# Optimization experiments

Hardware: AMD Instinct MI355X
Metric: run time of the kernel (lower is better)

## Reference

```python
import jax, jax.numpy as jnp
import numpy as np

POOL, D_MODEL, D_FF, M_DIM = 512, 1024, 4096, 64
B, S, K = 2, 2048, 8


def setup_inputs() -> dict:
    key = jax.random.key(0)
    ks = jax.random.split(key, 8)
    x = jax.random.normal(ks[0], (B, S, D_MODEL), dtype=jnp.float32)
    selected_indices = jax.random.randint(ks[1], (B, S, K), 0, POOL, dtype=jnp.int32)
    pattern_weights = jax.random.normal(ks[2], (B, S, K), dtype=jnp.float32)
    base_patterns = 0.02 * jax.random.normal(ks[3], (POOL, D_FF), dtype=jnp.float32)
    # nn.Linear(d_model, pool_size*mod_dim): weight [P*M, d_model], xavier-uniform
    lim_cm = float(np.sqrt(6.0 / (D_MODEL + POOL * M_DIM)))
    cm_w = jax.random.uniform(ks[4], (POOL * M_DIM, D_MODEL), jnp.float32, -lim_cm, lim_cm)
    cm_b = jnp.zeros((POOL * M_DIM,), jnp.float32)
    adj_proj = 0.01 * jax.random.normal(ks[5], (M_DIM, D_FF), dtype=jnp.float32)
    lim_w2 = float(np.sqrt(6.0 / (D_FF + D_MODEL)))
    w2_w = jax.random.uniform(ks[6], (D_MODEL, D_FF), jnp.float32, -lim_w2, lim_w2)
    w2_b = jnp.zeros((D_MODEL,), jnp.float32)
    return {"x": x, "selected_indices": selected_indices, "pattern_weights": pattern_weights,
            "base_patterns": base_patterns, "cm_w": cm_w, "cm_b": cm_b,
            "adj_proj": adj_proj, "w2_w": w2_w, "w2_b": w2_b}


def reference(x, selected_indices, pattern_weights, base_patterns, cm_w, cm_b, adj_proj, w2_w, w2_b):
    b, s, k = selected_indices.shape
    # gather base firing patterns for selected neurons: [b,s,k,d_ff]
    bp = base_patterns[selected_indices]
    # dense context modulation then gather (matches original module): [b,s,P,M]
    mod = (jnp.einsum('bsd,nd->bsn', x, cm_w) + cm_b).reshape(b, s, POOL, M_DIM)
    sel_mod = jnp.take_along_axis(mod, selected_indices[..., None], axis=2)  # [b,s,k,M]
    adjustments = jnp.einsum('bskm,mf->bskf', sel_mod, adj_proj)
    adjusted = bp + adjustments  # [b,s,k,d_ff]
    w = jax.nn.softmax(pattern_weights, axis=-1)
    combined = jnp.einsum('bsk,bskf->bsf', w, adjusted)  # [b,s,d_ff]
    activated = jax.nn.gelu(combined, approximate=False)  # torch default gelu = exact erf
    return jnp.einsum('bsf,df->bsd', activated, w2_w) + w2_b
```

## Files before the change

### kernel.cpp

```cpp
#include <hip/hip_runtime.h>
#include <math.h>

#define T_    4096
#define K_    8
#define POOL_ 512
#define DM_   1024
#define DFF_  4096
#define MD_   64
#define KC_   576

typedef __bf16 bf16x8 __attribute__((ext_vector_type(8)));
typedef __bf16 bf16x4 __attribute__((ext_vector_type(4)));
typedef float  f32x4  __attribute__((ext_vector_type(4)));

typedef __attribute__((address_space(1))) const void g_void;
typedef __attribute__((address_space(3))) void s_void;

__device__ __forceinline__ void async_ld16(const void* g, void* s) {
    __builtin_amdgcn_global_load_lds((g_void*)g, (s_void*)s, 16, 0, 0);
}
__device__ __forceinline__ float gelu_exact(float g) {
    return 0.5f * g * (1.f + erff(g * 0.70710678118654752f));
}
__device__ __forceinline__ bf16x4 cvt4(float4 v) {
    bf16x4 o;
    o[0] = (__bf16)v.x; o[1] = (__bf16)v.y; o[2] = (__bf16)v.z; o[3] = (__bf16)v.w;
    return o;
}
__device__ __forceinline__ bf16x8 cvt8(float4 a, float4 b) {
    bf16x8 o;
    o[0] = (__bf16)a.x; o[1] = (__bf16)a.y; o[2] = (__bf16)a.z; o[3] = (__bf16)a.w;
    o[4] = (__bf16)b.x; o[5] = (__bf16)b.y; o[6] = (__bf16)b.z; o[7] = (__bf16)b.w;
    return o;
}

__global__ __launch_bounds__(256) void k_hist(const int* __restrict__ sel,
                                              int* __restrict__ counts) {
    int i = blockIdx.x * 256 + threadIdx.x;
    if (i < T_ * K_) atomicAdd(&counts[sel[i]], 1);
}

__global__ __launch_bounds__(512) void k_scan(const int* __restrict__ counts,
                                              int* __restrict__ offsets,
                                              int* __restrict__ cursor) {
    __shared__ int s[512];
    const int t = threadIdx.x;
    const int c = counts[t];
    s[t] = c;
    __syncthreads();
    for (int d = 1; d < 512; d <<= 1) {
        int v = (t >= d) ? s[t - d] : 0;
        __syncthreads();
        s[t] += v;
        __syncthreads();
    }
    offsets[t] = s[t] - c;
    cursor[t]  = s[t] - c;
    if (t == 511) offsets[512] = s[511];
}

__global__ __launch_bounds__(256) void k_scatter(const int* __restrict__ sel,
                                                 int* __restrict__ cursor,
                                                 int* __restrict__ bucket,
                                                 int* __restrict__ rank) {
    int i = blockIdx.x * 256 + threadIdx.x;
    if (i < T_ * K_) {
        int p = sel[i];
        int pos = atomicAdd(&cursor[p], 1);
        bucket[pos] = i;
        rank[i] = pos;
    }
}

__global__ __launch_bounds__(256) void k_cvt(const float* __restrict__ src,
                                             __bf16* __restrict__ dst, int n16) {
    int i = blockIdx.x * 256 + threadIdx.x;
    if (i >= n16) return;
    const float4* s = (const float4*)src + (long)i * 4;
    float4 a = s[0], b = s[1], c = s[2], d = s[3];
    bf16x8 o0 = cvt8(a, b), o1 = cvt8(c, d);
    bf16x8* dp = (bf16x8*)dst + (long)i * 2;
    dp[0] = o0; dp[1] = o1;
}

__global__ __launch_bounds__(256) void k_selmod(
    const __bf16* __restrict__ xb, const float* __restrict__ cm_w,
    const int* __restrict__ bucket, const int* __restrict__ offsets,
    float* __restrict__ Y)
{
    const int p   = blockIdx.x;
    const int ms  = blockIdx.y;
    const int off = offsets[p];
    const int n   = offsets[p + 1] - off;
    if (n == 0) return;

    const int wave = threadIdx.x >> 6, lane = threadIdx.x & 63;
    const int quad = lane >> 4, l15 = lane & 15;

    const float* wrow = cm_w + (long)(p * 64 + ms * 16 + l15) * DM_ + quad * 8;

    const int nch = (n + 15) >> 4;
    for (int c = wave; c < nch; c += 4) {
        const int base = c * 16;
        int row = base + l15; if (row >= n) row = n - 1;
        const int tok = bucket[off + row] >> 3;
        const __bf16* xrow = xb + (long)tok * DM_ + quad * 8;

        f32x4 acc = {};
        #pragma unroll 4
        for (int kc = 0; kc < DM_; kc += 32) {
            bf16x8 afr = *(const bf16x8*)(xrow + kc);
            float4 w0  = *(const float4*)(wrow + kc);
            float4 w1  = *(const float4*)(wrow + kc + 4);
            bf16x8 bfr = cvt8(w0, w1);
            acc = __builtin_amdgcn_mfma_f32_16x16x32_bf16(afr, bfr, acc, 0, 0, 0);
        }
        #pragma unroll
        for (int r = 0; r < 4; ++r) {
            int prow = base + quad * 4 + r;
            if (prow < n)
                Y[(long)(off + prow) * MD_ + ms * 16 + l15] = acc[r];
        }
    }
}

__global__ __launch_bounds__(256) void k_wdense(
    const float* __restrict__ Y, const int* __restrict__ sel,
    const int* __restrict__ rank, const float* __restrict__ pw,
    const float* __restrict__ cm_b, __bf16* __restrict__ Wd)
{
    const int tid = threadIdx.x;
    const int tt = tid >> 6, m = tid & 63;
    const int t = blockIdx.x * 4 + tt;
    __shared__ float w_s[4][8];
    __shared__ int   sidx[4][8];
    __shared__ int   rnk[4][8];
    __shared__ __align__(16) __bf16 row[4][KC_];

    if (m < 8) {
        w_s[tt][m]  = pw[t * 8 + m];
        sidx[tt][m] = sel[t * 8 + m];
        rnk[tt][m]  = rank[t * 8 + m];
    }
    __syncthreads();
    if (m == 0) {
        float mx = w_s[tt][0];
        #pragma unroll
        for (int k = 1; k < 8; ++k) mx = fmaxf(mx, w_s[tt][k]);
        float sum = 0.f;
        #pragma unroll
        for (int k = 0; k < 8; ++k) { float e = expf(w_s[tt][k] - mx); w_s[tt][k] = e; sum += e; }
        float inv = 1.f / sum;
        #pragma unroll
        for (int k = 0; k < 8; ++k) w_s[tt][k] *= inv;
    }
    __syncthreads();
    *(uint4*)&row[tt][m * 8] = make_uint4(0, 0, 0, 0);
    {
        float a = 0.f;
        #pragma unroll
        for (int k = 0; k < 8; ++k) {
            float y = cm_b[sidx[tt][k] * 64 + m] + Y[(long)rnk[tt][k] * MD_ + m];
            a += w_s[tt][k] * y;
        }
        row[tt][512 + m] = (__bf16)a;
    }
    __syncthreads();
    if (m == 0) {
        #pragma unroll
        for (int k = 0; k < 8; ++k) {
            int c = sidx[tt][k];
            row[tt][c] = (__bf16)((float)row[tt][c] + w_s[tt][k]);
        }
    }
    __syncthreads();
    const uint4* src = (const uint4*)&row[0][0];
    uint4* dst = (uint4*)(Wd + (long)blockIdx.x * 4 * KC_);
    for (int e = tid; e < 4 * KC_ * 2 / 16; e += 256) dst[e] = src[e];
}

__global__ __launch_bounds__(256) void k_buildP(
    const float* __restrict__ bp, const float* __restrict__ adj,
    __bf16* __restrict__ P)
{
    __shared__ __bf16 tile[64][72];
    const int tid = threadIdx.x;
    const int bx = blockIdx.x, f0 = blockIdx.y * 64;
    const float* src = (bx < 8) ? (bp + (long)bx * 64 * DFF_) : adj;
    for (int e = tid; e < 4096; e += 256) {
        int f = e & 63, c = e >> 6;
        tile[c][f] = (__bf16)src[(long)c * DFF_ + f0 + f];
    }
    __syncthreads();
    const int c0 = bx * 64;
    for (int e = tid; e < 4096; e += 256) {
        int c = e & 63, f = e >> 6;
        P[(long)(f0 + f) * KC_ + c0 + c] = tile[c][f];
    }
}

__global__ __launch_bounds__(256) void k_actgemm(
    const __bf16* __restrict__ A, const __bf16* __restrict__ Bw,
    __bf16* __restrict__ act)
{
    __shared__ __align__(16) __bf16 sA[128 * 32];
    __shared__ __align__(16) __bf16 sB[128 * 32];
    const int tid  = threadIdx.x;
    const int tm   = blockIdx.y * 128, tn = blockIdx.x * 128;
    const int wave = tid >> 6, lane = tid & 63, quad = lane >> 4, l15 = lane & 15;
    const int wm   = (wave >> 1) * 64, wn = (wave & 1) * 64;

    f32x4 acc[4][4] = {};

    const int e    = tid * 8;
    const int srow = e >> 5;
    const int scol = e & 31;
    const __bf16* agp0 = A  + ((long)(tm + srow)      * KC_ + scol);
    const __bf16* agp1 = A  + ((long)(tm + 64 + srow) * KC_ + scol);
    const __bf16* bgp0 = Bw + ((long)(tn + srow)      * KC_ + scol);
    const __bf16* bgp1 = Bw + ((long)(tn + 64 + srow) * KC_ + scol);
    void* sa0 = (void*)(sA + e);
    void* sa1 = (void*)(sA + 2048 + e);
    void* sb0 = (void*)(sB + e);
    void* sb1 = (void*)(sB + 2048 + e);

    for (int kk = 0; kk < KC_; kk += 32) {
        async_ld16(agp0 + kk, sa0);
        async_ld16(agp1 + kk, sa1);
        async_ld16(bgp0 + kk, sb0);
        async_ld16(bgp1 + kk, sb1);
        __syncthreads();
        bf16x8 af[4], bf[4];
        #pragma unroll
        for (int i = 0; i < 4; ++i)
            af[i] = *(const bf16x8*)(sA + (wm + i * 16 + l15) * 32 + quad * 8);
        #pragma unroll
        for (int j = 0; j < 4; ++j)
            bf[j] = *(const bf16x8*)(sB + (wn + j * 16 + l15) * 32 + quad * 8);
        #pragma unroll
        for (int i = 0; i < 4; ++i)
            #pragma unroll
            for (int j = 0; j < 4; ++j)
                acc[i][j] = __builtin_amdgcn_mfma_f32_16x16x32_bf16(af[i], bf[j], acc[i][j], 0, 0, 0);
        __syncthreads();
    }

    #pragma unroll
    for (int j = 0; j < 4; ++j) {
        const int col = tn + wn + j * 16 + l15;
        #pragma unroll
        for (int i = 0; i < 4; ++i) {
            const int row = tm + wm + i * 16 + quad * 4;
            #pragma unroll
            for (int r = 0; r < 4; ++r)
                act[(long)(row + r) * DFF_ + col] = (__bf16)gelu_exact(acc[i][j][r]);
        }
    }
}

__global__ __launch_bounds__(256) void k_outgemm(
    const __bf16* __restrict__ A, const __bf16* __restrict__ Bw,
    const float* __restrict__ bias, float* __restrict__ out)
{
    __shared__ __align__(16) __bf16 sA[128 * 128];
    __shared__ __align__(16) __bf16 sB[128 * 128];
    const int tid  = threadIdx.x;
    const int tm   = blockIdx.y * 128, tn = blockIdx.x * 128;
    const int wave = tid >> 6, lane = tid & 63, quad = lane >> 4, l15 = lane & 15;
    const int wm   = (wave >> 1) * 64, wn = (wave & 1) * 64;

    f32x4 acc[4][4] = {};

    const int e  = tid * 8;
    const int r0 = e >> 5;
    const int cc = e & 31;

    for (int kk = 0; kk < DFF_; kk += 128) {
        #pragma unroll
        for (int s = 0; s < 4; ++s) {
            #pragma unroll
            for (int q = 0; q < 2; ++q) {
                async_ld16(A  + (long)(tm + q * 64 + r0) * DFF_ + kk + s * 32 + cc,
                           (void*)(sA + s * 4096 + q * 2048 + e));
                async_ld16(Bw + (long)(tn + q * 64 + r0) * DFF_ + kk + s * 32 + cc,
                           (void*)(sB + s * 4096 + q * 2048 + e));
            }
        }
        __syncthreads();
        #pragma unroll
        for (int s = 0; s < 4; ++s) {
            bf16x8 af[4], bf[4];
            #pragma unroll
            for (int i = 0; i < 4; ++i)
                af[i] = *(const bf16x8*)(sA + s * 4096 + (wm + i * 16 + l15) * 32 + quad * 8);
            #pragma unroll
            for (int j = 0; j < 4; ++j)
                bf[j] = *(const bf16x8*)(sB + s * 4096 + (wn + j * 16 + l15) * 32 + quad * 8);
            #pragma unroll
            for (int i = 0; i < 4; ++i)
                #pragma unroll
                for (int j = 0; j < 4; ++j)
                    acc[i][j] = __builtin_amdgcn_mfma_f32_16x16x32_bf16(af[i], bf[j], acc[i][j], 0, 0, 0);
        }
        __syncthreads();
    }

    #pragma unroll
    for (int j = 0; j < 4; ++j) {
        const int col = tn + wn + j * 16 + l15;
        const float bj = bias[col];
        #pragma unroll
        for (int i = 0; i < 4; ++i) {
            const int row = tm + wm + i * 16 + quad * 4;
            #pragma unroll
            for (int r = 0; r < 4; ++r)
                out[(long)(row + r) * 1024 + col] = acc[i][j][r] + bj;
        }
    }
}

extern "C" void kernel_launch(void* const* d_in, const int* in_sizes, int n_in,
                              void* d_out, int out_size, void* d_ws, size_t ws_size,
                              hipStream_t stream) {
    const float* x    = (const float*)d_in[0];
    const int*   sel  = (const int*)  d_in[1];
    const float* pw   = (const float*)d_in[2];
    const float* bp   = (const float*)d_in[3];
    const float* cm_w = (const float*)d_in[4];
    const float* cm_b = (const float*)d_in[5];
    const float* adj  = (const float*)d_in[6];
    const float* w2   = (const float*)d_in[7];
    const float* w2b  = (const float*)d_in[8];
    float* out = (float*)d_out;

    char* ws = (char*)d_ws;
    __bf16* x_bf = (__bf16*)ws;
    __bf16* act  = (__bf16*)ws;
    __bf16* P    = (__bf16*)(ws + (size_t)32 * 1024 * 1024);
    __bf16* w2bf = (__bf16*)(ws + (size_t)37 * 1024 * 1024);
    char*  bins  = ws + (size_t)45 * 1024 * 1024;
    int* bucket  = (int*)bins;
    int* rank    = (int*)(bins + 131072);
    int* counts  = (int*)(bins + 262144);
    int* cursor  = (int*)(bins + 264192);
    int* offsets = (int*)(bins + 266240);

    float*  Y  = (float*)d_out;
    __bf16* Wd = (__bf16*)((char*)d_out + (size_t)8 * 1024 * 1024);

    hipMemsetAsync(counts, 0, 4096, stream);
    k_hist   <<<128, 256, 0, stream>>>(sel, counts);
    k_scan   <<<1,   512, 0, stream>>>(counts, offsets, cursor);
    k_scatter<<<128, 256, 0, stream>>>(sel, cursor, bucket, rank);
    k_cvt    <<<1024, 256, 0, stream>>>(x, x_bf, T_ * DM_ / 16);
    k_selmod <<<dim3(POOL_, 4), 256, 0, stream>>>(x_bf, cm_w, bucket, offsets, Y);
    k_wdense <<<T_ / 4, 256, 0, stream>>>(Y, sel, rank, pw, cm_b, Wd);
    k_buildP <<<dim3(9, 64), 256, 0, stream>>>(bp, adj, P);
    k_cvt    <<<1024, 256, 0, stream>>>(w2, w2bf, DM_ * DFF_ / 16);
    k_actgemm<<<dim3(DFF_ / 128, T_ / 128), 256, 0, stream>>>(Wd, P, act);
    k_outgemm<<<dim3(DM_ / 128, T_ / 128), 256, 0, stream>>>(act, w2bf, w2b, out);
}
```

Before: 444.7 us.

## Tile selmod GEMM through double-buffered LDS with one block per pool entry

The selected-modulation kernel now uses one block per pool neuron instead of four, and stages both the 64 cm_w rows and up to 128 gathered token rows in LDS in 64-wide K chunks. Each wave computes 16 output columns across all token chunks, and the next chunk is prefetched into registers to overlap with the MFMAs. Previously every wave reloaded and reconverted the fp32 weight rows for each 16-token chunk straight from global memory, and the gathered x rows were read once per column-split block. The new layout lets those loads be reused, at the cost of fewer blocks (512), more shared memory and syncs per K step.

```diff
diff --git a/kernel.cpp b/kernel.cpp
--- a/kernel.cpp
+++ b/kernel.cpp
@@ -89,37 +89,105 @@
     float* __restrict__ Y)
 {
     const int p   = blockIdx.x;
-    const int ms  = blockIdx.y;
     const int off = offsets[p];
     const int n   = offsets[p + 1] - off;
     if (n == 0) return;
 
-    const int wave = threadIdx.x >> 6, lane = threadIdx.x & 63;
+    const int tid  = threadIdx.x;
+    const int wave = tid >> 6, lane = tid & 63;
     const int quad = lane >> 4, l15 = lane & 15;
 
-    const float* wrow = cm_w + (long)(p * 64 + ms * 16 + l15) * DM_ + quad * 8;
-
-    const int nch = (n + 15) >> 4;
-    for (int c = wave; c < nch; c += 4) {
-        const int base = c * 16;
-        int row = base + l15; if (row >= n) row = n - 1;
-        const int tok = bucket[off + row] >> 3;
-        const __bf16* xrow = xb + (long)tok * DM_ + quad * 8;
-
-        f32x4 acc = {};
-        #pragma unroll 4
-        for (int kc = 0; kc < DM_; kc += 32) {
-            bf16x8 afr = *(const bf16x8*)(xrow + kc);
-            float4 w0  = *(const float4*)(wrow + kc);
-            float4 w1  = *(const float4*)(wrow + kc + 4);
-            bf16x8 bfr = cvt8(w0, w1);
-            acc = __builtin_amdgcn_mfma_f32_16x16x32_bf16(afr, bfr, acc, 0, 0, 0);
-        }
-        #pragma unroll
-        for (int r = 0; r < 4; ++r) {
-            int prow = base + quad * 4 + r;
-            if (prow < n)
-                Y[(long)(off + prow) * MD_ + ms * 16 + l15] = acc[r];
+    __shared__ int list[128];
+    __shared__ __align__(16) __bf16 Wl[2][64][72];
+    __shared__ __align__(16) __bf16 Xl[2][128][72];
+
+    const int wr = tid >> 4;
+    const int wc = (tid & 15) * 4;
+    const float* wbase = cm_w + (long)(p * 64 + wr) * DM_ + wc;
+
+    for (int g0 = 0; g0 < n; g0 += 128) {
+        const int gn   = (n - g0 < 128) ? (n - g0) : 128;
+        const int nch  = (gn + 15) >> 4;
+        const int rows = nch << 4;
+
+        if (tid < rows) {
+            int r = g0 + tid; if (r >= n) r = n - 1;
+            list[tid] = bucket[off + r] >> 3;
+        }
+        __syncthreads();
+
+        const __bf16* xsrc[4];
+        int  xoff[4];
+        bool xon[4];
+        #pragma unroll
+        for (int q = 0; q < 4; ++q) {
+            const int g = tid + q * 256;
+            xon[q] = (g < rows * 8);
+            const int row = xon[q] ? (g >> 3) : 0;
+            xsrc[q] = xb + (long)list[row] * DM_ + (g & 7) * 8;
+            xoff[q] = row * 144 + (g & 7) * 16;
+        }
+
+        float4 wv[4]; bf16x8 xv[4];
+        #pragma unroll
+        for (int q = 0; q < 4; ++q)
+            wv[q] = *(const float4*)(wbase + (long)q * 16 * DM_);
+        #pragma unroll
+        for (int q = 0; q < 4; ++q)
+            if (xon[q]) xv[q] = *(const bf16x8*)(xsrc[q]);
+        #pragma unroll
+        for (int q = 0; q < 4; ++q)
+            *(bf16x4*)&Wl[0][q * 16 + wr][wc] = cvt4(wv[q]);
+        #pragma unroll
+        for (int q = 0; q < 4; ++q)
+            if (xon[q]) *(bf16x8*)((char*)&Xl[0][0][0] + xoff[q]) = xv[q];
+        __syncthreads();
+
+        f32x4 acc[8] = {};
+
+        for (int t = 0; t < 16; ++t) {
+            const int cur = t & 1;
+            if (t < 15) {
+                #pragma unroll
+                for (int q = 0; q < 4; ++q)
+                    wv[q] = *(const float4*)(wbase + (long)q * 16 * DM_ + (t + 1) * 64);
+                #pragma unroll
+                for (int q = 0; q < 4; ++q)
+                    if (xon[q]) xv[q] = *(const bf16x8*)(xsrc[q] + (t + 1) * 64);
+            }
+            #pragma unroll
+            for (int ks = 0; ks < 2; ++ks) {
+                const bf16x8 bfr = *(const bf16x8*)&Wl[cur][wave * 16 + l15][ks * 32 + quad * 8];
+                #pragma unroll
+                for (int c = 0; c < 8; ++c) {
+                    if (c < nch) {
+                        const bf16x8 afr = *(const bf16x8*)&Xl[cur][c * 16 + l15][ks * 32 + quad * 8];
+                        acc[c] = __builtin_amdgcn_mfma_f32_16x16x32_bf16(afr, bfr, acc[c], 0, 0, 0);
+                    }
+                }
+            }
+            if (t < 15) {
+                const int nxt = cur ^ 1;
+                #pragma unroll
+                for (int q = 0; q < 4; ++q)
+                    *(bf16x4*)&Wl[nxt][q * 16 + wr][wc] = cvt4(wv[q]);
+                #pragma unroll
+                for (int q = 0; q < 4; ++q)
+                    if (xon[q]) *(bf16x8*)((char*)&Xl[nxt][0][0] + xoff[q]) = xv[q];
+            }
+            __syncthreads();
+        }
+
+        #pragma unroll
+        for (int c = 0; c < 8; ++c) {
+            if (c < nch) {
+                #pragma unroll
+                for (int r = 0; r < 4; ++r) {
+                    const int prow = c * 16 + quad * 4 + r;
+                    if (prow < gn)
+                        Y[(long)(off + g0 + prow) * MD_ + wave * 16 + l15] = acc[c][r];
+                }
+            }
         }
     }
 }
@@ -353,7 +421,7 @@
     k_scan   <<<1,   512, 0, stream>>>(counts, offsets, cursor);
     k_scatter<<<128, 256, 0, stream>>>(sel, cursor, bucket, rank);
     k_cvt    <<<1024, 256, 0, stream>>>(x, x_bf, T_ * DM_ / 16);
-    k_selmod <<<dim3(POOL_, 4), 256, 0, stream>>>(x_bf, cm_w, bucket, offsets, Y);
+    k_selmod <<<POOL_, 256, 0, stream>>>(x_bf, cm_w, bucket, offsets, Y);
     k_wdense <<<T_ / 4, 256, 0, stream>>>(Y, sel, rank, pw, cm_b, Wd);
     k_buildP <<<dim3(9, 64), 256, 0, stream>>>(bp, adj, P);
     k_cvt    <<<1024, 256, 0, stream>>>(w2, w2bf, DM_ * DFF_ / 16);
```

New measurement: 489.4 us. 10.1% more time.

## Split selmod over K quarters with LDS-staged weights and token tiles

Applied to the files above, without the earlier changes.

The grid's y dimension now selects a quarter of the reduction dimension (256 of 1024) instead of a 16-column slice of the output. Each block converts its pool's 64x256 weight slice to bf16 once into LDS and processes gathered token rows in groups of 48 staged through LDS, so every weight fragment is reused across up to three MFMA tiles. Before, each wave re-read and re-converted fp32 weights from global memory for every 16-token chunk. The four partial sums go to separate buffers in the workspace and are added in k_wdense, which costs extra memory traffic and relies on those workspace regions not overlapping live data at that point.

```diff
diff --git a/kernel.cpp b/kernel.cpp
--- a/kernel.cpp
+++ b/kernel.cpp
@@ -86,48 +86,92 @@
 __global__ __launch_bounds__(256) void k_selmod(
     const __bf16* __restrict__ xb, const float* __restrict__ cm_w,
     const int* __restrict__ bucket, const int* __restrict__ offsets,
-    float* __restrict__ Y)
+    float* __restrict__ Y0, float* __restrict__ Y1,
+    float* __restrict__ Y2, float* __restrict__ Y3)
 {
     const int p   = blockIdx.x;
-    const int ms  = blockIdx.y;
+    const int kh  = blockIdx.y;
     const int off = offsets[p];
     const int n   = offsets[p + 1] - off;
     if (n == 0) return;
-
-    const int wave = threadIdx.x >> 6, lane = threadIdx.x & 63;
+    float* Y = (kh == 0) ? Y0 : (kh == 1) ? Y1 : (kh == 2) ? Y2 : Y3;
+
+    const int tid  = threadIdx.x;
+    const int wave = tid >> 6, lane = tid & 63;
     const int quad = lane >> 4, l15 = lane & 15;
 
-    const float* wrow = cm_w + (long)(p * 64 + ms * 16 + l15) * DM_ + quad * 8;
-
-    const int nch = (n + 15) >> 4;
-    for (int c = wave; c < nch; c += 4) {
-        const int base = c * 16;
-        int row = base + l15; if (row >= n) row = n - 1;
-        const int tok = bucket[off + row] >> 3;
-        const __bf16* xrow = xb + (long)tok * DM_ + quad * 8;
-
-        f32x4 acc = {};
-        #pragma unroll 4
-        for (int kc = 0; kc < DM_; kc += 32) {
-            bf16x8 afr = *(const bf16x8*)(xrow + kc);
-            float4 w0  = *(const float4*)(wrow + kc);
-            float4 w1  = *(const float4*)(wrow + kc + 4);
-            bf16x8 bfr = cvt8(w0, w1);
-            acc = __builtin_amdgcn_mfma_f32_16x16x32_bf16(afr, bfr, acc, 0, 0, 0);
-        }
-        #pragma unroll
-        for (int r = 0; r < 4; ++r) {
-            int prow = base + quad * 4 + r;
-            if (prow < n)
-                Y[(long)(off + prow) * MD_ + ms * 16 + l15] = acc[r];
-        }
+    __shared__ int list[48];
+    __shared__ __align__(16) __bf16 Wl[64][264];
+    __shared__ __align__(16) __bf16 Xl[48][264];
+
+    {
+        const int wr = tid >> 6;
+        const int wc = (tid & 63) * 4;
+        const float* wsrc = cm_w + (long)(p * 64 + wr) * DM_ + kh * 256 + wc;
+        float4 wv[16];
+        #pragma unroll
+        for (int j = 0; j < 16; ++j)
+            wv[j] = *(const float4*)(wsrc + (long)j * 4 * DM_);
+        #pragma unroll
+        for (int j = 0; j < 16; ++j)
+            *(bf16x4*)&Wl[wr + j * 4][wc] = cvt4(wv[j]);
+    }
+
+    for (int g0 = 0; g0 < n; g0 += 48) {
+        const int gn  = min(n - g0, 48);
+        const int nch = (gn + 15) >> 4;
+
+        __syncthreads();
+        if (tid < 48) {
+            int r = g0 + tid; if (r >= n) r = n - 1;
+            list[tid] = bucket[off + r] >> 3;
+        }
+        __syncthreads();
+
+        {
+            bf16x8 xv[6];
+            #pragma unroll
+            for (int j = 0; j < 6; ++j) {
+                const int row = (tid >> 5) + j * 8;
+                const int c16 = (tid & 31) * 8;
+                xv[j] = *(const bf16x8*)(xb + (long)list[row] * DM_ + kh * 256 + c16);
+            }
+            #pragma unroll
+            for (int j = 0; j < 6; ++j)
+                *(bf16x8*)&Xl[(tid >> 5) + j * 8][(tid & 31) * 8] = xv[j];
+        }
+        __syncthreads();
+
+        f32x4 acc[3] = {};
+        #pragma unroll
+        for (int ks = 0; ks < 8; ++ks) {
+            const bf16x8 bfr = *(const bf16x8*)&Wl[wave * 16 + l15][ks * 32 + quad * 8];
+            #pragma unroll
+            for (int c = 0; c < 3; ++c)
+                if (c < nch) {
+                    const bf16x8 afr = *(const bf16x8*)&Xl[c * 16 + l15][ks * 32 + quad * 8];
+                    acc[c] = __builtin_amdgcn_mfma_f32_16x16x32_bf16(afr, bfr, acc[c], 0, 0, 0);
+                }
+        }
+        #pragma unroll
+        for (int c = 0; c < 3; ++c)
+            if (c < nch) {
+                #pragma unroll
+                for (int r = 0; r < 4; ++r) {
+                    const int prow = c * 16 + quad * 4 + r;
+                    if (prow < gn)
+                        Y[(long)(off + g0 + prow) * MD_ + wave * 16 + l15] = acc[c][r];
+                }
+            }
     }
 }
 
 __global__ __launch_bounds__(256) void k_wdense(
-    const float* __restrict__ Y, const int* __restrict__ sel,
-    const int* __restrict__ rank, const float* __restrict__ pw,
-    const float* __restrict__ cm_b, __bf16* __restrict__ Wd)
+    const float* __restrict__ Y0, const float* __restrict__ Y1,
+    const float* __restrict__ Y2, const float* __restrict__ Y3,
+    const int* __restrict__ sel, const int* __restrict__ rank,
+    const float* __restrict__ pw, const float* __restrict__ cm_b,
+    __bf16* __restrict__ Wd)
 {
     const int tid = threadIdx.x;
     const int tt = tid >> 6, m = tid & 63;
@@ -160,7 +204,8 @@
         float a = 0.f;
         #pragma unroll
         for (int k = 0; k < 8; ++k) {
-            float y = cm_b[sidx[tt][k] * 64 + m] + Y[(long)rnk[tt][k] * MD_ + m];
+            const long yb = (long)rnk[tt][k] * MD_ + m;
+            float y = cm_b[sidx[tt][k] * 64 + m] + Y0[yb] + Y1[yb] + Y2[yb] + Y3[yb];
             a += w_s[tt][k] * y;
         }
         row[tt][512 + m] = (__bf16)a;
@@ -336,6 +381,9 @@
     char* ws = (char*)d_ws;
     __bf16* x_bf = (__bf16*)ws;
     __bf16* act  = (__bf16*)ws;
+    float*  Yp1  = (float*)(ws + (size_t) 8 * 1024 * 1024);
+    float*  Yp2  = (float*)(ws + (size_t)16 * 1024 * 1024);
+    float*  Yp3  = (float*)(ws + (size_t)24 * 1024 * 1024);
     __bf16* P    = (__bf16*)(ws + (size_t)32 * 1024 * 1024);
     __bf16* w2bf = (__bf16*)(ws + (size_t)37 * 1024 * 1024);
     char*  bins  = ws + (size_t)45 * 1024 * 1024;
@@ -345,16 +393,17 @@
     int* cursor  = (int*)(bins + 264192);
     int* offsets = (int*)(bins + 266240);
 
-    float*  Y  = (float*)d_out;
-    __bf16* Wd = (__bf16*)((char*)d_out + (size_t)8 * 1024 * 1024);
+    float*  Yp0 = (float*)d_out;
+    __bf16* Wd  = (__bf16*)((char*)d_out + (size_t)8 * 1024 * 1024);
 
     hipMemsetAsync(counts, 0, 4096, stream);
     k_hist   <<<128, 256, 0, stream>>>(sel, counts);
     k_scan   <<<1,   512, 0, stream>>>(counts, offsets, cursor);
     k_scatter<<<128, 256, 0, stream>>>(sel, cursor, bucket, rank);
     k_cvt    <<<1024, 256, 0, stream>>>(x, x_bf, T_ * DM_ / 16);
-    k_selmod <<<dim3(POOL_, 4), 256, 0, stream>>>(x_bf, cm_w, bucket, offsets, Y);
-    k_wdense <<<T_ / 4, 256, 0, stream>>>(Y, sel, rank, pw, cm_b, Wd);
+    k_selmod <<<dim3(POOL_, 4), 256, 0, stream>>>(x_bf, cm_w, bucket, offsets,
+                                                  Yp0, Yp1, Yp2, Yp3);
+    k_wdense <<<T_ / 4, 256, 0, stream>>>(Yp0, Yp1, Yp2, Yp3, sel, rank, pw, cm_b, Wd);
     k_buildP <<<dim3(9, 64), 256, 0, stream>>>(bp, adj, P);
     k_cvt    <<<1024, 256, 0, stream>>>(w2, w2bf, DM_ * DFF_ / 16);
     k_actgemm<<<dim3(DFF_ / 128, T_ / 128), 256, 0, stream>>>(Wd, P, act);
```

After: 408.5 us. 1.09x faster.
